# Kernel optimization log

Hardware: AMD Instinct MI355X
Metric: run time of the kernel (lower is better)

The kernel has to match this reference:

```python
import jax, jax.numpy as jnp
import numpy as np
from jax import lax


def rgb2hsl(rgb):
    # rgb: [B,3,H,W] in [0,1]
    cmax = jnp.max(rgb, axis=1, keepdims=True)
    cmin = jnp.min(rgb, axis=1, keepdims=True)
    amax = jnp.argmax(rgb, axis=1, keepdims=True)  # first-occurrence, like torch.max
    delta = cmax - cmin
    idx = jnp.where(delta == 0, 3, amax)
    safe_d = jnp.where(delta == 0, 1.0, delta)
    r, g, b = rgb[:, 0:1], rgb[:, 1:2], rgb[:, 2:3]
    h0 = jnp.mod((g - b) / safe_d, 6.0)
    h1 = (b - r) / safe_d + 2.0
    h2 = (r - g) / safe_d + 4.0
    hsl_h = jnp.where(idx == 0, h0,
            jnp.where(idx == 1, h1,
            jnp.where(idx == 2, h2, 0.0))) / 6.0
    hsl_l = (cmax + cmin) / 2.0
    # s = delta/(2l) if l<=0.5 else delta/(2-2l); 0 at l==0 or l==1
    denom = jnp.where(hsl_l <= 0.5, 2.0 * hsl_l, 2.0 - 2.0 * hsl_l)
    safe_den = jnp.where(denom == 0, 1.0, denom)
    in_range = (hsl_l > 0) & (hsl_l < 1)
    hsl_s = jnp.where(in_range, delta / safe_den, 0.0)
    return jnp.concatenate([hsl_h, hsl_s, hsl_l], axis=1)


def conv2d_same(x, w, b):
    y = lax.conv_general_dilated(x, w, window_strides=(1, 1), padding='SAME',
                                 dimension_numbers=('NCHW', 'OIHW', 'NCHW'))
    return y + b[None, :, None, None]


def setup_inputs() -> dict:
    key = jax.random.key(0)
    k = jax.random.split(key, 5)
    B, H, W = 32, 512, 512
    KS = 5
    fan1 = 1 * KS * KS
    fan2 = 2 * KS * KS
    return {
        'x': jax.random.uniform(k[0], (B, 3, H, W), dtype=jnp.float32),
        'w1': jax.random.normal(k[1], (3, 1, KS, KS), dtype=jnp.float32) / np.sqrt(fan1),
        'b1': jax.random.normal(k[2], (3,), dtype=jnp.float32) * 0.01,
        'w2': jax.random.normal(k[3], (3, 2, KS, KS), dtype=jnp.float32) / np.sqrt(fan2),
        'b2': jax.random.normal(k[4], (3,), dtype=jnp.float32) * 0.01,
    }


def reference(x, w1, b1, w2, b2):
    x_hsl = rgb2hsl(x)
    xl = conv2d_same(x_hsl[:, 2:3], w1, b1)   # L plane -> conv1
    xr = conv2d_same(x_hsl[:, 0:2], w2, b2)   # H,S planes -> conv2
    return (xl, xr)
```

## Files before the change

### kernel.cpp

```cpp
#include <hip/hip_runtime.h>

typedef _Float16 h2 __attribute__((ext_vector_type(2)));

__device__ __forceinline__ float fd2(unsigned a, unsigned b, float c) {
  return __builtin_amdgcn_fdot2(__builtin_bit_cast(h2, a), __builtin_bit_cast(h2, b), c, false);
}
__device__ __forceinline__ unsigned pkrtz(float a, float b) {
  return __builtin_bit_cast(unsigned, __builtin_amdgcn_cvt_pkrtz(a, b));
}

#define TW 64
#define TH 32
#define ROWS 36
#define SWW 84
#define SLW 88
#define NT 4

__global__ __launch_bounds__(256, 4) void fused_hsl_conv(
    const float* __restrict__ x,
    const float* __restrict__ w1,
    const float* __restrict__ b1,
    const float* __restrict__ w2,
    const float* __restrict__ b2,
    float* __restrict__ out,
    int B)
{
  __shared__ unsigned sHS[2][ROWS][SWW];
  __shared__ __align__(16) _Float16 sL[2][ROWS][SLW];
  __shared__ unsigned swHS[5][16];
  __shared__ unsigned swL[5][16];

  const int tid = threadIdx.x;

  if (tid < 15) {
    const int o = tid % 3, dy = tid / 3;
    #pragma unroll
    for (int dx = 0; dx < 5; ++dx)
      swHS[dy][o * 5 + dx] = pkrtz(w2[o * 50 + dy * 5 + dx],
                                   w2[o * 50 + 25 + dy * 5 + dx]);
  } else if (tid >= 32 && tid < 47) {
    const int t2 = tid - 32, o = t2 % 3, dy = t2 / 3;
    float wv[5];
    #pragma unroll
    for (int dx = 0; dx < 5; ++dx) wv[dx] = w1[o * 25 + dy * 5 + dx];
    swL[dy][o * 3 + 0] = pkrtz(wv[0], wv[1]);
    swL[dy][o * 3 + 1] = pkrtz(wv[2], wv[3]);
    swL[dy][o * 3 + 2] = pkrtz(wv[4], 0.f);
  } else if (tid >= 64 && tid < 69) {
    swHS[tid - 64][15] = 0;
  } else if (tid >= 96 && tid < 131) {
    const int t3 = tid - 96;
    swL[t3 / 7][9 + t3 % 7] = 0;
  }
  if (tid < 72) {
    const int r = tid >> 1, w = 34 + (tid & 1);
    ((unsigned*)&sL[0][r][0])[w] = 0;
    ((unsigned*)&sL[1][r][0])[w] = 0;
  }

  const int nwg = gridDim.x;
  const int bsw = (blockIdx.x & 7) * (nwg >> 3) + (blockIdx.x >> 3);
  const int b   = bsw >> 5;
  const int rem = bsw & 31;
  const int tx0 = (rem & 7) * TW;
  const int tyb = (rem >> 3) * (NT * TH);

  const size_t pln = 512 * 512;
  const float* pr = x + (size_t)b * 3 * pln;
  const float* pg = pr + pln;
  const float* pb = pg + pln;
  float* outl = out + (size_t)b * 3 * pln;
  float* outr = out + ((size_t)B + b) * 3 * pln;

  const float b1v0 = b1[0], b1v1 = b1[1], b1v2 = b1[2];
  const float b2v0 = b2[0], b2v1 = b2[1], b2v2 = b2[2];

  const bool act = tid < 216;
  int rowA[3], tA[3];
  #pragma unroll
  for (int k = 0; k < 3; ++k) {
    const int i = k * 216 + tid;
    rowA[k] = i / 18;
    tA[k]   = i - rowA[k] * 18;
  }

  auto issue_loads = [&](int ty0, float4* Rv, float4* Gv, float4* Bv) {
    #pragma unroll
    for (int k = 0; k < 3; ++k) {
      const int gy  = ty0 - 2 + rowA[k];
      const int gx0 = tx0 - 4 + 4 * tA[k];
      Rv[k] = make_float4(0.f, 0.f, 0.f, 0.f);
      Gv[k] = Rv[k]; Bv[k] = Rv[k];
      if (act && gy >= 0 && gy < 512 && gx0 >= 0 && gx0 < 512) {
        const size_t off = (size_t)gy * 512 + gx0;
        Rv[k] = *(const float4*)(pr + off);
        Gv[k] = *(const float4*)(pg + off);
        Bv[k] = *(const float4*)(pb + off);
      }
    }
  };

  auto convert_store = [&](int buf, const float4* Rv, const float4* Gv, const float4* Bv) {
    #pragma unroll
    for (int k = 0; k < 3; ++k) {
      const int row = rowA[k], t = tA[k];
      const float ra[4] = {Rv[k].x, Rv[k].y, Rv[k].z, Rv[k].w};
      const float ga[4] = {Gv[k].x, Gv[k].y, Gv[k].z, Gv[k].w};
      const float ba[4] = {Bv[k].x, Bv[k].y, Bv[k].z, Bv[k].w};
      unsigned hs[4]; _Float16 lv[4];
      #pragma unroll
      for (int p = 0; p < 4; ++p) {
        const float r = ra[p], g = ga[p], bl = ba[p];
        const float cmax = fmaxf(r, fmaxf(g, bl));
        const float cmin = fminf(r, fminf(g, bl));
        const float delta = cmax - cmin;
        const float l = 0.5f * (cmax + cmin);
        const float rd = __builtin_amdgcn_rcpf(delta);
        float h0 = (g - bl) * rd;
        h0 = (h0 < 0.f) ? h0 + 6.f : h0;
        const float h1v = (bl - r) * rd + 2.f;
        const float h2v = (r - g) * rd + 4.f;
        float hv = (r >= g && r >= bl) ? h0 : ((g >= bl) ? h1v : h2v);
        const float h = (delta != 0.f) ? hv * (1.f / 6.f) : 0.f;
        const float denom = (l <= 0.5f) ? (2.f * l) : (2.f - 2.f * l);
        const float s = (delta != 0.f && l > 0.f && l < 1.f)
                          ? delta * __builtin_amdgcn_rcpf(denom) : 0.f;
        hs[p] = pkrtz(h, s);
        lv[p] = (_Float16)l;
      }
      if (act) {
        if (t >= 1)  *(uint2*)&sHS[buf][row][4 * t - 2] = make_uint2(hs[0], hs[1]);
        if (t <= 16) *(uint2*)&sHS[buf][row][4 * t]     = make_uint2(hs[2], hs[3]);
        unsigned* rl = (unsigned*)&sL[buf][row][0];
        if (t >= 1)  rl[2 * t - 1] = __builtin_bit_cast(unsigned, (h2){lv[0], lv[1]});
        if (t <= 16) rl[2 * t]     = __builtin_bit_cast(unsigned, (h2){lv[2], lv[3]});
      }
    }
  };

  const int lx = tid & 7;
  const int ly = tid >> 3;
  const int q0 = 8 * lx;

  float4 Rv[3], Gv[3], Bv[3];
  issue_loads(tyb, Rv, Gv, Bv);
  convert_store(0, Rv, Gv, Bv);
  __syncthreads();

  for (int it = 0; it < NT; ++it) {
    const int ty0 = tyb + it * TH;
    const int buf = it & 1;

    float4 Rn[3], Gn[3], Bn[3];
    if (it + 1 < NT) issue_loads(ty0 + TH, Rn, Gn, Bn);

    const size_t ob = (size_t)(ty0 + ly) * 512 + (tx0 + q0);

    {
      float acc[3][8];
      #pragma unroll
      for (int p = 0; p < 8; ++p) { acc[0][p] = b2v0; acc[1][p] = b2v1; acc[2][p] = b2v2; }
      #pragma unroll
      for (int dy = 0; dy < 5; ++dy) {
        const unsigned* rowp = &sHS[buf][ly + dy][0];
        const uint4 A0 = *(const uint4*)(rowp + q0);
        const uint4 A1 = *(const uint4*)(rowp + q0 + 4);
        const uint4 A2 = *(const uint4*)(rowp + q0 + 8);
        const unsigned hw[12] = {A0.x, A0.y, A0.z, A0.w, A1.x, A1.y, A1.z, A1.w,
                                 A2.x, A2.y, A2.z, A2.w};
        const uint4 W0 = *(const uint4*)&swHS[dy][0];
        const uint4 W1 = *(const uint4*)&swHS[dy][4];
        const uint4 W2 = *(const uint4*)&swHS[dy][8];
        const uint4 W3 = *(const uint4*)&swHS[dy][12];
        const unsigned wt[15] = {W0.x, W0.y, W0.z, W0.w, W1.x, W1.y, W1.z, W1.w,
                                 W2.x, W2.y, W2.z, W2.w, W3.x, W3.y, W3.z};
        #pragma unroll
        for (int o = 0; o < 3; ++o)
          #pragma unroll
          for (int p = 0; p < 8; ++p)
            #pragma unroll
            for (int dx = 0; dx < 5; ++dx)
              acc[o][p] = fd2(hw[p + dx], wt[o * 5 + dx], acc[o][p]);
      }
      #pragma unroll
      for (int o = 0; o < 3; ++o) {
        *(float4*)(outr + o * pln + ob)     = make_float4(acc[o][0], acc[o][1], acc[o][2], acc[o][3]);
        *(float4*)(outr + o * pln + ob + 4) = make_float4(acc[o][4], acc[o][5], acc[o][6], acc[o][7]);
      }
    }

    {
      float acc[3][8];
      #pragma unroll
      for (int p = 0; p < 8; ++p) { acc[0][p] = b1v0; acc[1][p] = b1v1; acc[2][p] = b1v2; }
      #pragma unroll
      for (int dy = 0; dy < 5; ++dy) {
        const unsigned* rowp = (const unsigned*)&sL[buf][ly + dy][0];
        const uint4 L0 = *(const uint4*)(rowp + 4 * lx);
        const uint4 L1 = *(const uint4*)(rowp + 4 * lx + 4);
        const unsigned w[8] = {L0.x, L0.y, L0.z, L0.w, L1.x, L1.y, L1.z, L1.w};
        unsigned s[6];
        #pragma unroll
        for (int k = 0; k < 6; ++k)
          s[k] = __builtin_amdgcn_alignbit(w[k + 1], w[k], 16);
        const uint4 V0 = *(const uint4*)&swL[dy][0];
        const uint4 V1 = *(const uint4*)&swL[dy][4];
        const unsigned c8 = swL[dy][8];
        const unsigned wt[9] = {V0.x, V0.y, V0.z, V0.w, V1.x, V1.y, V1.z, V1.w, c8};
        #pragma unroll
        for (int o = 0; o < 3; ++o)
          #pragma unroll
          for (int p = 0; p < 8; ++p) {
            const int hh = p >> 1;
            const unsigned* src = (p & 1) ? s : w;
            acc[o][p] = fd2(src[hh],     wt[o * 3 + 0], acc[o][p]);
            acc[o][p] = fd2(src[hh + 1], wt[o * 3 + 1], acc[o][p]);
            acc[o][p] = fd2(src[hh + 2], wt[o * 3 + 2], acc[o][p]);
          }
      }
      #pragma unroll
      for (int o = 0; o < 3; ++o) {
        *(float4*)(outl + o * pln + ob)     = make_float4(acc[o][0], acc[o][1], acc[o][2], acc[o][3]);
        *(float4*)(outl + o * pln + ob + 4) = make_float4(acc[o][4], acc[o][5], acc[o][6], acc[o][7]);
      }
    }

    if (it + 1 < NT) convert_store(buf ^ 1, Rn, Gn, Bn);
    __syncthreads();
  }
}

extern "C" void kernel_launch(void* const* d_in, const int* in_sizes, int n_in,
                              void* d_out, int out_size, void* d_ws, size_t ws_size,
                              hipStream_t stream) {
  const float* x  = (const float*)d_in[0];
  const float* w1 = (const float*)d_in[1];
  const float* b1 = (const float*)d_in[2];
  const float* w2 = (const float*)d_in[3];
  const float* b2 = (const float*)d_in[4];
  float* out = (float*)d_out;

  const int B = in_sizes[0] / (3 * 512 * 512);
  const int grid = B * 32;
  fused_hsl_conv<<<grid, 256, 0, stream>>>(x, w1, b1, w2, b2, out, B);
}
```

Before: 73.41 us.

## Split workgroup into dedicated producer wave and consumer waves for conv tiles

Adds a fifth wavefront (threads 256-319) that alone loads the next RGB tile from global memory, converts it to HSL and stores it into the alternate LDS buffer. The 256 consumer threads now only run the two convolutions, so they no longer carry in-flight prefetch registers or do the conversion work. The intent is to overlap global loads and conversion with compute through warp specialization. In exchange, one wave must load and convert 11 float4 triples per thread, which may make it the critical path. The block size rises to 320, which changes occupancy, and the per-iteration barrier becomes a hand-written s_waitcnt plus s_barrier.

```diff
diff --git a/kernel.cpp b/kernel.cpp
--- a/kernel.cpp
+++ b/kernel.cpp
@@ -7,6 +7,10 @@
 }
 __device__ __forceinline__ unsigned pkrtz(float a, float b) {
   return __builtin_bit_cast(unsigned, __builtin_amdgcn_cvt_pkrtz(a, b));
+}
+
+__device__ __forceinline__ void wg_barrier_lds() {
+  asm volatile("s_waitcnt lgkmcnt(0)\n\ts_barrier" ::: "memory");
 }
 
 #define TW 64
@@ -16,7 +20,7 @@
 #define SLW 88
 #define NT 4
 
-__global__ __launch_bounds__(256, 4) void fused_hsl_conv(
+__global__ __launch_bounds__(320, 5) void fused_hsl_conv(
     const float* __restrict__ x,
     const float* __restrict__ w1,
     const float* __restrict__ b1,
@@ -72,63 +76,54 @@
   float* outl = out + (size_t)b * 3 * pln;
   float* outr = out + ((size_t)B + b) * 3 * pln;
 
-  const float b1v0 = b1[0], b1v1 = b1[1], b1v2 = b1[2];
-  const float b2v0 = b2[0], b2v1 = b2[1], b2v2 = b2[2];
-
-  const bool act = tid < 216;
-  int rowA[3], tA[3];
-  #pragma unroll
-  for (int k = 0; k < 3; ++k) {
-    const int i = k * 216 + tid;
-    rowA[k] = i / 18;
-    tA[k]   = i - rowA[k] * 18;
-  }
-
-  auto issue_loads = [&](int ty0, float4* Rv, float4* Gv, float4* Bv) {
-    #pragma unroll
-    for (int k = 0; k < 3; ++k) {
-      const int gy  = ty0 - 2 + rowA[k];
-      const int gx0 = tx0 - 4 + 4 * tA[k];
-      Rv[k] = make_float4(0.f, 0.f, 0.f, 0.f);
-      Gv[k] = Rv[k]; Bv[k] = Rv[k];
-      if (act && gy >= 0 && gy < 512 && gx0 >= 0 && gx0 < 512) {
+  const bool isProd = tid >= 256;
+  const int  pl = tid - 256;
+
+  auto stage = [&](int ty0, int buf) {
+    float4 PR[11], PG[11], PB[11];
+    #pragma unroll
+    for (int j = 0; j < 11; ++j) {
+      const int i = pl + 64 * j;
+      const int row = i / 18, t = i - row * 18;
+      const int gy = ty0 - 2 + row, gx0 = tx0 - 4 + 4 * t;
+      PR[j] = make_float4(0.f, 0.f, 0.f, 0.f);
+      PG[j] = PR[j]; PB[j] = PR[j];
+      if (i < 648 && gy >= 0 && gy < 512 && gx0 >= 0 && gx0 < 512) {
         const size_t off = (size_t)gy * 512 + gx0;
-        Rv[k] = *(const float4*)(pr + off);
-        Gv[k] = *(const float4*)(pg + off);
-        Bv[k] = *(const float4*)(pb + off);
+        PR[j] = *(const float4*)(pr + off);
+        PG[j] = *(const float4*)(pg + off);
+        PB[j] = *(const float4*)(pb + off);
       }
     }
-  };
-
-  auto convert_store = [&](int buf, const float4* Rv, const float4* Gv, const float4* Bv) {
-    #pragma unroll
-    for (int k = 0; k < 3; ++k) {
-      const int row = rowA[k], t = tA[k];
-      const float ra[4] = {Rv[k].x, Rv[k].y, Rv[k].z, Rv[k].w};
-      const float ga[4] = {Gv[k].x, Gv[k].y, Gv[k].z, Gv[k].w};
-      const float ba[4] = {Bv[k].x, Bv[k].y, Bv[k].z, Bv[k].w};
-      unsigned hs[4]; _Float16 lv[4];
-      #pragma unroll
-      for (int p = 0; p < 4; ++p) {
-        const float r = ra[p], g = ga[p], bl = ba[p];
-        const float cmax = fmaxf(r, fmaxf(g, bl));
-        const float cmin = fminf(r, fminf(g, bl));
-        const float delta = cmax - cmin;
-        const float l = 0.5f * (cmax + cmin);
-        const float rd = __builtin_amdgcn_rcpf(delta);
-        float h0 = (g - bl) * rd;
-        h0 = (h0 < 0.f) ? h0 + 6.f : h0;
-        const float h1v = (bl - r) * rd + 2.f;
-        const float h2v = (r - g) * rd + 4.f;
-        float hv = (r >= g && r >= bl) ? h0 : ((g >= bl) ? h1v : h2v);
-        const float h = (delta != 0.f) ? hv * (1.f / 6.f) : 0.f;
-        const float denom = (l <= 0.5f) ? (2.f * l) : (2.f - 2.f * l);
-        const float s = (delta != 0.f && l > 0.f && l < 1.f)
-                          ? delta * __builtin_amdgcn_rcpf(denom) : 0.f;
-        hs[p] = pkrtz(h, s);
-        lv[p] = (_Float16)l;
-      }
-      if (act) {
+    #pragma unroll
+    for (int j = 0; j < 11; ++j) {
+      const int i = pl + 64 * j;
+      if (i < 648) {
+        const int row = i / 18, t = i - row * 18;
+        const float ra[4] = {PR[j].x, PR[j].y, PR[j].z, PR[j].w};
+        const float ga[4] = {PG[j].x, PG[j].y, PG[j].z, PG[j].w};
+        const float ba[4] = {PB[j].x, PB[j].y, PB[j].z, PB[j].w};
+        unsigned hs[4]; _Float16 lv[4];
+        #pragma unroll
+        for (int p = 0; p < 4; ++p) {
+          const float r = ra[p], g = ga[p], bl = ba[p];
+          const float cmax = fmaxf(r, fmaxf(g, bl));
+          const float cmin = fminf(r, fminf(g, bl));
+          const float delta = cmax - cmin;
+          const float l = 0.5f * (cmax + cmin);
+          const float rd = __builtin_amdgcn_rcpf(delta);
+          float h0 = (g - bl) * rd;
+          h0 = (h0 < 0.f) ? h0 + 6.f : h0;
+          const float h1v = (bl - r) * rd + 2.f;
+          const float h2v = (r - g) * rd + 4.f;
+          float hv = (r >= g && r >= bl) ? h0 : ((g >= bl) ? h1v : h2v);
+          const float h = (delta != 0.f) ? hv * (1.f / 6.f) : 0.f;
+          const float denom = (l <= 0.5f) ? (2.f * l) : (2.f - 2.f * l);
+          const float s = (delta != 0.f && l > 0.f && l < 1.f)
+                            ? delta * __builtin_amdgcn_rcpf(denom) : 0.f;
+          hs[p] = pkrtz(h, s);
+          lv[p] = (_Float16)l;
+        }
         if (t >= 1)  *(uint2*)&sHS[buf][row][4 * t - 2] = make_uint2(hs[0], hs[1]);
         if (t <= 16) *(uint2*)&sHS[buf][row][4 * t]     = make_uint2(hs[2], hs[3]);
         unsigned* rl = (unsigned*)&sL[buf][row][0];
@@ -142,91 +137,92 @@
   const int ly = tid >> 3;
   const int q0 = 8 * lx;
 
-  float4 Rv[3], Gv[3], Bv[3];
-  issue_loads(tyb, Rv, Gv, Bv);
-  convert_store(0, Rv, Gv, Bv);
+  const float b1v0 = b1[0], b1v1 = b1[1], b1v2 = b1[2];
+  const float b2v0 = b2[0], b2v1 = b2[1], b2v2 = b2[2];
+
+  if (isProd) stage(tyb, 0);
   __syncthreads();
 
   for (int it = 0; it < NT; ++it) {
+    const int buf = it & 1;
     const int ty0 = tyb + it * TH;
-    const int buf = it & 1;
-
-    float4 Rn[3], Gn[3], Bn[3];
-    if (it + 1 < NT) issue_loads(ty0 + TH, Rn, Gn, Bn);
-
-    const size_t ob = (size_t)(ty0 + ly) * 512 + (tx0 + q0);
-
-    {
-      float acc[3][8];
-      #pragma unroll
-      for (int p = 0; p < 8; ++p) { acc[0][p] = b2v0; acc[1][p] = b2v1; acc[2][p] = b2v2; }
-      #pragma unroll
-      for (int dy = 0; dy < 5; ++dy) {
-        const unsigned* rowp = &sHS[buf][ly + dy][0];
-        const uint4 A0 = *(const uint4*)(rowp + q0);
-        const uint4 A1 = *(const uint4*)(rowp + q0 + 4);
-        const uint4 A2 = *(const uint4*)(rowp + q0 + 8);
-        const unsigned hw[12] = {A0.x, A0.y, A0.z, A0.w, A1.x, A1.y, A1.z, A1.w,
-                                 A2.x, A2.y, A2.z, A2.w};
-        const uint4 W0 = *(const uint4*)&swHS[dy][0];
-        const uint4 W1 = *(const uint4*)&swHS[dy][4];
-        const uint4 W2 = *(const uint4*)&swHS[dy][8];
-        const uint4 W3 = *(const uint4*)&swHS[dy][12];
-        const unsigned wt[15] = {W0.x, W0.y, W0.z, W0.w, W1.x, W1.y, W1.z, W1.w,
-                                 W2.x, W2.y, W2.z, W2.w, W3.x, W3.y, W3.z};
-        #pragma unroll
-        for (int o = 0; o < 3; ++o)
+
+    if (!isProd) {
+      const size_t ob = (size_t)(ty0 + ly) * 512 + (tx0 + q0);
+
+      {
+        float acc[3][8];
+        #pragma unroll
+        for (int p = 0; p < 8; ++p) { acc[0][p] = b2v0; acc[1][p] = b2v1; acc[2][p] = b2v2; }
+        #pragma unroll
+        for (int dy = 0; dy < 5; ++dy) {
+          const unsigned* rowp = &sHS[buf][ly + dy][0];
+          const uint4 A0 = *(const uint4*)(rowp + q0);
+          const uint4 A1 = *(const uint4*)(rowp + q0 + 4);
+          const uint4 A2 = *(const uint4*)(rowp + q0 + 8);
+          const unsigned hw[12] = {A0.x, A0.y, A0.z, A0.w, A1.x, A1.y, A1.z, A1.w,
+                                   A2.x, A2.y, A2.z, A2.w};
+          const uint4 W0 = *(const uint4*)&swHS[dy][0];
+          const uint4 W1 = *(const uint4*)&swHS[dy][4];
+          const uint4 W2 = *(const uint4*)&swHS[dy][8];
+          const uint4 W3 = *(const uint4*)&swHS[dy][12];
+          const unsigned wt[15] = {W0.x, W0.y, W0.z, W0.w, W1.x, W1.y, W1.z, W1.w,
+                                   W2.x, W2.y, W2.z, W2.w, W3.x, W3.y, W3.z};
           #pragma unroll
-          for (int p = 0; p < 8; ++p)
+          for (int o = 0; o < 3; ++o)
             #pragma unroll
-            for (int dx = 0; dx < 5; ++dx)
-              acc[o][p] = fd2(hw[p + dx], wt[o * 5 + dx], acc[o][p]);
-      }
-      #pragma unroll
-      for (int o = 0; o < 3; ++o) {
-        *(float4*)(outr + o * pln + ob)     = make_float4(acc[o][0], acc[o][1], acc[o][2], acc[o][3]);
-        *(float4*)(outr + o * pln + ob + 4) = make_float4(acc[o][4], acc[o][5], acc[o][6], acc[o][7]);
-      }
+            for (int p = 0; p < 8; ++p)
+              #pragma unroll
+              for (int dx = 0; dx < 5; ++dx)
+                acc[o][p] = fd2(hw[p + dx], wt[o * 5 + dx], acc[o][p]);
+        }
+        #pragma unroll
+        for (int o = 0; o < 3; ++o) {
+          *(float4*)(outr + o * pln + ob)     = make_float4(acc[o][0], acc[o][1], acc[o][2], acc[o][3]);
+          *(float4*)(outr + o * pln + ob + 4) = make_float4(acc[o][4], acc[o][5], acc[o][6], acc[o][7]);
+        }
+      }
+
+      {
+        float acc[3][8];
+        #pragma unroll
+        for (int p = 0; p < 8; ++p) { acc[0][p] = b1v0; acc[1][p] = b1v1; acc[2][p] = b1v2; }
+        #pragma unroll
+        for (int dy = 0; dy < 5; ++dy) {
+          const unsigned* rowp = (const unsigned*)&sL[buf][ly + dy][0];
+          const uint4 L0 = *(const uint4*)(rowp + 4 * lx);
+          const uint4 L1 = *(const uint4*)(rowp + 4 * lx + 4);
+          const unsigned w[8] = {L0.x, L0.y, L0.z, L0.w, L1.x, L1.y, L1.z, L1.w};
+          unsigned s[6];
+          #pragma unroll
+          for (int k = 0; k < 6; ++k)
+            s[k] = __builtin_amdgcn_alignbit(w[k + 1], w[k], 16);
+          const uint4 V0 = *(const uint4*)&swL[dy][0];
+          const uint4 V1 = *(const uint4*)&swL[dy][4];
+          const unsigned c8 = swL[dy][8];
+          const unsigned wt[9] = {V0.x, V0.y, V0.z, V0.w, V1.x, V1.y, V1.z, V1.w, c8};
+          #pragma unroll
+          for (int o = 0; o < 3; ++o)
+            #pragma unroll
+            for (int p = 0; p < 8; ++p) {
+              const int hh = p >> 1;
+              const unsigned* src = (p & 1) ? s : w;
+              acc[o][p] = fd2(src[hh],     wt[o * 3 + 0], acc[o][p]);
+              acc[o][p] = fd2(src[hh + 1], wt[o * 3 + 1], acc[o][p]);
+              acc[o][p] = fd2(src[hh + 2], wt[o * 3 + 2], acc[o][p]);
+            }
+        }
+        #pragma unroll
+        for (int o = 0; o < 3; ++o) {
+          *(float4*)(outl + o * pln + ob)     = make_float4(acc[o][0], acc[o][1], acc[o][2], acc[o][3]);
+          *(float4*)(outl + o * pln + ob + 4) = make_float4(acc[o][4], acc[o][5], acc[o][6], acc[o][7]);
+        }
+      }
+    } else {
+      if (it + 1 < NT) stage(ty0 + TH, buf ^ 1);
     }
 
-    {
-      float acc[3][8];
-      #pragma unroll
-      for (int p = 0; p < 8; ++p) { acc[0][p] = b1v0; acc[1][p] = b1v1; acc[2][p] = b1v2; }
-      #pragma unroll
-      for (int dy = 0; dy < 5; ++dy) {
-        const unsigned* rowp = (const unsigned*)&sL[buf][ly + dy][0];
-        const uint4 L0 = *(const uint4*)(rowp + 4 * lx);
-        const uint4 L1 = *(const uint4*)(rowp + 4 * lx + 4);
-        const unsigned w[8] = {L0.x, L0.y, L0.z, L0.w, L1.x, L1.y, L1.z, L1.w};
-        unsigned s[6];
-        #pragma unroll
-        for (int k = 0; k < 6; ++k)
-          s[k] = __builtin_amdgcn_alignbit(w[k + 1], w[k], 16);
-        const uint4 V0 = *(const uint4*)&swL[dy][0];
-        const uint4 V1 = *(const uint4*)&swL[dy][4];
-        const unsigned c8 = swL[dy][8];
-        const unsigned wt[9] = {V0.x, V0.y, V0.z, V0.w, V1.x, V1.y, V1.z, V1.w, c8};
-        #pragma unroll
-        for (int o = 0; o < 3; ++o)
-          #pragma unroll
-          for (int p = 0; p < 8; ++p) {
-            const int hh = p >> 1;
-            const unsigned* src = (p & 1) ? s : w;
-            acc[o][p] = fd2(src[hh],     wt[o * 3 + 0], acc[o][p]);
-            acc[o][p] = fd2(src[hh + 1], wt[o * 3 + 1], acc[o][p]);
-            acc[o][p] = fd2(src[hh + 2], wt[o * 3 + 2], acc[o][p]);
-          }
-      }
-      #pragma unroll
-      for (int o = 0; o < 3; ++o) {
-        *(float4*)(outl + o * pln + ob)     = make_float4(acc[o][0], acc[o][1], acc[o][2], acc[o][3]);
-        *(float4*)(outl + o * pln + ob + 4) = make_float4(acc[o][4], acc[o][5], acc[o][6], acc[o][7]);
-      }
-    }
-
-    if (it + 1 < NT) convert_store(buf ^ 1, Rn, Gn, Bn);
-    __syncthreads();
+    if (it + 1 < NT) wg_barrier_lds();
   }
 }
 
@@ -242,5 +238,5 @@
 
   const int B = in_sizes[0] / (3 * 512 * 512);
   const int grid = B * 32;
-  fused_hsl_conv<<<grid, 256, 0, stream>>>(x, w1, b1, w2, b2, out, B);
-}
+  fused_hsl_conv<<<grid, 320, 0, stream>>>(x, w1, b1, w2, b2, out, B);
+}
```

Measured after the change: 265.7 us. +262.0%, slower.
